# Optimization experiments

Measured on AMD Instinct MI355X. Metric: run time of the kernel, lower is better.

## Reference

```python
import jax, jax.numpy as jnp
import numpy as np
from jax import lax

FUSE_EPOCH = 9
STRIDE = (1, 1)
PAD = [(1, 1), (1, 1)]


def _conv_one(xi, ki):
    # xi: [ic, H, W], ki: [oc, ic, ks, ks] -> [oc, H', W']
    return lax.conv_general_dilated(
        xi[None], ki, window_strides=STRIDE, padding=PAD,
        dimension_numbers=("NCHW", "OIHW", "NCHW"))[0]


def setup_inputs() -> dict:
    key = jax.random.key(0)
    k1, k2, k3, k4 = jax.random.split(key, 4)
    B, IC, OC, KS, H, W, NDEMOG = 64, 64, 64, 3, 112, 112, 4
    x = jax.random.normal(k1, (B, IC, H, W), dtype=jnp.float32)
    fan_in = IC * KS * KS
    kernel_base = jax.random.normal(k2, (OC, IC, KS, KS), dtype=jnp.float32) / np.sqrt(fan_in)
    kernel_mask = jax.random.normal(k3, (NDEMOG, IC, KS, KS), dtype=jnp.float32)
    demog_label = jax.random.randint(k4, (B,), 0, NDEMOG, dtype=jnp.int64)
    return {"x": x, "kernel_base": kernel_base, "kernel_mask": kernel_mask,
            "demog_label": demog_label, "epoch": 0}


def reference(x, kernel_base, kernel_mask, demog_label, epoch):
    # Original: for each demog group d, conv samples with label d using
    # kernel_base * kernel_mask[d], scatter into output. Equivalent to a
    # per-sample kernel gathered by label (fuse_mark == -1 path uses mask 0
    # when epoch >= fuse_epoch).
    if epoch >= FUSE_EPOCH:
        idx = jnp.zeros_like(demog_label)
    else:
        idx = demog_label
    # per-sample kernels: [B, oc, ic, ks, ks]
    kernels = kernel_base[None] * kernel_mask[idx][:, None]
    return jax.vmap(_conv_one)(x, kernels)
```

## Files before the change

kernel.cpp:

```cpp
#include <hip/hip_runtime.h>
#include <hip/hip_bf16.h>


#define HH 112
#define WW 112
#define ICn 64
#define OCn 64
#define FUSE_EPOCH 9
#define NPIX (HH * WW)

typedef __attribute__((ext_vector_type(8)))  short  short8;
typedef __attribute__((ext_vector_type(8)))  unsigned short bf8;
typedef __attribute__((ext_vector_type(16))) float  f32x16;
typedef unsigned int u32;

#define WF_BYTES ((size_t)4 * 64 * 576 * 2)

static __device__ __forceinline__ unsigned short f2bf(float v) {
    __hip_bfloat16 hb = __float2bfloat16(v);
    return *reinterpret_cast<unsigned short*>(&hb);
}

static __device__ __forceinline__ void gload16(const unsigned short* g, unsigned short* l) {
    __builtin_amdgcn_global_load_lds(
        (const __attribute__((address_space(1))) u32*)g,
        (__attribute__((address_space(3))) u32*)l, 16, 0, 0);
}

__global__ __launch_bounds__(256)
void fuse_w_kernel(const float* __restrict__ kb, const float* __restrict__ km,
                   unsigned short* __restrict__ wf2)
{
    int idx = blockIdx.x * 256 + threadIdx.x;
    if (idx >= 4 * 4 * 9 * 2 * 64 * 8) return;
    int e  = idx & 7;
    int oc = (idx >> 3) & 63;
    int h  = (idx >> 9) & 1;
    int r  = idx >> 10;
    int t  = r % 9; r /= 9;
    int ck = r & 3;
    int d  = r >> 2;
    int ic = ck * 16 + h * 8 + e;
    wf2[idx] = f2bf(kb[(oc * ICn + ic) * 9 + t] * km[(d * ICn + ic) * 9 + t]);
}

__global__ __launch_bounds__(256, 2)
void adaconv_fused(const float* __restrict__ x,
                   const unsigned short* __restrict__ wf2,
                   const int* __restrict__ label,
                   const int* __restrict__ epoch,
                   float* __restrict__ out)
{
    __shared__ unsigned short Bb[2][10944];
    __shared__ unsigned short Ab[2][9216];

    const int tid  = threadIdx.x;
    const int b    = blockIdx.y;
    const int y0   = blockIdx.x * 4;
    const int w    = tid >> 6;
    const int lane = tid & 63;
    const int ln   = lane & 31;
    const int h    = lane >> 5;

    int d = (epoch[0] >= FUSE_EPOCH) ? 0 : label[b];
    d &= 3;
    const unsigned short* wfd = wf2 + (size_t)d * 36864;

    const float* ga[12];
    int  lbase[3];
    bool wact[3], gval[3];
    #pragma unroll
    for (int r = 0; r < 3; ++r) {
        int c = r * 256 + tid;
        bool a = (c < 672);
        int cc = a ? c : 671;
        int seg = cc % 28;
        int q   = cc / 28;
        int icq = q & 1;
        int rh  = q >> 1;
        int lr  = rh >> 1;
        int hh  = rh & 1;
        int gy  = y0 - 1 + lr;
        bool v  = ((unsigned)gy < 112u);
        wact[r] = a;
        gval[r] = v;
        lbase[r] = (rh * 114 + 4 * seg + 1) * 8 + icq * 4;
        int icl = hh * 8 + icq * 4;
        #pragma unroll
        for (int i = 0; i < 4; ++i)
            ga[r * 4 + i] = x + ((size_t)(b * 64 + icl + i) * 112 + (v ? gy : 0)) * 112 + 4 * seg;
    }

    auto issueA = [&](int buf, int ck1) {
        #pragma unroll
        for (int r = 0; r < 5; ++r) {
            int c = r * 256 + tid;
            if (c < 1152)
                gload16(wfd + ck1 * 9216 + (size_t)c * 8, &Ab[buf][(r * 256 + w * 64) * 8]);
        }
    };

    f32x16 acc[2][4];
    #pragma unroll
    for (int m = 0; m < 2; ++m)
        #pragma unroll
        for (int j = 0; j < 4; ++j)
            #pragma unroll
            for (int k = 0; k < 16; ++k) acc[m][j][k] = 0.f;

    const int bb = (w * 228 + h * 114 + ln) * 8;
    const int ab = h * 512 + ln * 8;

    if (tid < 48) {
        int bz = tid / 24, z = tid % 24;
        int rh = z >> 1, px = (z & 1) ? 113 : 0;
        bf8 zz = bf8{0,0,0,0,0,0,0,0};
        *reinterpret_cast<bf8*>(&Bb[bz][(rh * 114 + px) * 8]) = zz;
    }
    {
        float4 vl[12];
        #pragma unroll
        for (int r = 0; r < 3; ++r)
            if (wact[r])
                #pragma unroll
                for (int i = 0; i < 4; ++i)
                    vl[r * 4 + i] = *reinterpret_cast<const float4*>(ga[r * 4 + i]);
        issueA(0, 0);
        #pragma unroll
        for (int r = 0; r < 3; ++r) {
            if (!wact[r]) continue;
            float c0[4] = {vl[r*4+0].x, vl[r*4+0].y, vl[r*4+0].z, vl[r*4+0].w};
            float c1[4] = {vl[r*4+1].x, vl[r*4+1].y, vl[r*4+1].z, vl[r*4+1].w};
            float c2[4] = {vl[r*4+2].x, vl[r*4+2].y, vl[r*4+2].z, vl[r*4+2].w};
            float c3[4] = {vl[r*4+3].x, vl[r*4+3].y, vl[r*4+3].z, vl[r*4+3].w};
            #pragma unroll
            for (int p = 0; p < 4; ++p) {
                float f0 = gval[r] ? c0[p] : 0.f;
                float f1 = gval[r] ? c1[p] : 0.f;
                float f2 = gval[r] ? c2[p] : 0.f;
                float f3 = gval[r] ? c3[p] : 0.f;
                __hip_bfloat162 u01 = __float22bfloat162_rn(make_float2(f0, f1));
                __hip_bfloat162 u23 = __float22bfloat162_rn(make_float2(f2, f3));
                uint2 wv;
                wv.x = *reinterpret_cast<unsigned*>(&u01);
                wv.y = *reinterpret_cast<unsigned*>(&u23);
                *reinterpret_cast<uint2*>(&Bb[0][lbase[r] + p * 8]) = wv;
            }
        }
        __syncthreads();
    }

    #pragma unroll
    for (int ck = 0; ck < 4; ++ck) {
        const int cur = ck & 1, nxt = cur ^ 1;
        float4 vl[12];
        if (ck < 3) {
            #pragma unroll
            for (int r = 0; r < 3; ++r)
                if (wact[r])
                    #pragma unroll
                    for (int i = 0; i < 4; ++i)
                        vl[r * 4 + i] = *reinterpret_cast<const float4*>(
                            ga[r * 4 + i] + (size_t)(ck + 1) * 200704);
            issueA(nxt, ck + 1);
            __builtin_amdgcn_sched_barrier(0);
        }

        const unsigned short* Bc = Bb[cur];
        const unsigned short* Ac = Ab[cur];
        #pragma unroll
        for (int kh = 0; kh < 3; ++kh) {
            #pragma unroll
            for (int kw = 0; kw < 3; ++kw) {
                const int t = kh * 3 + kw;
                short8 a0 = *reinterpret_cast<const short8*>(&Ac[ab + t * 1024]);
                short8 a1 = *reinterpret_cast<const short8*>(&Ac[ab + 256 + t * 1024]);
                #pragma unroll
                for (int j = 0; j < 4; ++j) {
                    short8 bj = *reinterpret_cast<const short8*>(
                        &Bc[bb + (kh * 228 + kw + j * 32) * 8]);
                    acc[0][j] = __builtin_amdgcn_mfma_f32_32x32x16_bf16(a0, bj, acc[0][j], 0, 0, 0);
                    acc[1][j] = __builtin_amdgcn_mfma_f32_32x32x16_bf16(a1, bj, acc[1][j], 0, 0, 0);
                }
            }
        }

        if (ck < 3) {
            #pragma unroll
            for (int r = 0; r < 3; ++r) {
                if (!wact[r]) continue;
                float c0[4] = {vl[r*4+0].x, vl[r*4+0].y, vl[r*4+0].z, vl[r*4+0].w};
                float c1[4] = {vl[r*4+1].x, vl[r*4+1].y, vl[r*4+1].z, vl[r*4+1].w};
                float c2[4] = {vl[r*4+2].x, vl[r*4+2].y, vl[r*4+2].z, vl[r*4+2].w};
                float c3[4] = {vl[r*4+3].x, vl[r*4+3].y, vl[r*4+3].z, vl[r*4+3].w};
                #pragma unroll
                for (int p = 0; p < 4; ++p) {
                    float f0 = gval[r] ? c0[p] : 0.f;
                    float f1 = gval[r] ? c1[p] : 0.f;
                    float f2 = gval[r] ? c2[p] : 0.f;
                    float f3 = gval[r] ? c3[p] : 0.f;
                    __hip_bfloat162 u01 = __float22bfloat162_rn(make_float2(f0, f1));
                    __hip_bfloat162 u23 = __float22bfloat162_rn(make_float2(f2, f3));
                    uint2 wv;
                    wv.x = *reinterpret_cast<unsigned*>(&u01);
                    wv.y = *reinterpret_cast<unsigned*>(&u23);
                    *reinterpret_cast<uint2*>(&Bb[nxt][lbase[r] + p * 8]) = wv;
                }
            }
        }
        __syncthreads();
    }

    #pragma unroll
    for (int m = 0; m < 2; ++m) {
        #pragma unroll
        for (int j = 0; j < 4; ++j) {
            if (j == 3 && ln >= 16) continue;
            float* ob = out + ((size_t)(b * OCn + m * 32 + 4 * h)) * NPIX
                            + (y0 + w) * WW + j * 32 + ln;
            #pragma unroll
            for (int reg = 0; reg < 16; ++reg) {
                int row = (reg & 3) + 8 * (reg >> 2);
                ob[(size_t)row * NPIX] = acc[m][j][reg];
            }
        }
    }
}

#define ICP 24
#define WSTRIDE 152
__global__ __launch_bounds__(256, 2)
void adaconv_fallback(const float* __restrict__ x,
                      const float* __restrict__ kb,
                      const float* __restrict__ km,
                      const int* __restrict__ label,
                      const int* __restrict__ epoch,
                      float* __restrict__ out)
{
    __shared__ unsigned short Xs[18][34][ICP];
    __shared__ unsigned short Ws[64][WSTRIDE];

    const int tid = threadIdx.x;
    const int b   = blockIdx.y;
    const int bx  = blockIdx.x & 3;
    const int byy = blockIdx.x >> 2;
    const int x0 = bx * 32, y0 = byy * 16;

    int d = (epoch[0] >= FUSE_EPOCH) ? 0 : label[b];
    d &= 3;

    const int w    = tid >> 6;
    const int lane = tid & 63;
    const int ln   = lane & 31;
    const int h    = lane >> 5;

    f32x16 acc[2][4];
    #pragma unroll
    for (int m = 0; m < 2; ++m)
        #pragma unroll
        for (int j = 0; j < 4; ++j)
            #pragma unroll
            for (int k = 0; k < 16; ++k) acc[m][j][k] = 0.f;

    const float* xb = x + (size_t)b * ICn * HH * WW;

    for (int ck = 0; ck < 4; ++ck) {
        const int icb = ck * 16;
        __syncthreads();
        for (int idx = tid; idx < 18 * 34 * 16; idx += 256) {
            int ic  = idx / 612;
            int rem = idx - ic * 612;
            int r   = rem / 34;
            int c   = rem - r * 34;
            int gy = y0 - 1 + r, gx = x0 - 1 + c;
            float v = 0.f;
            if ((unsigned)gy < HH && (unsigned)gx < WW)
                v = xb[(size_t)(icb + ic) * (HH * WW) + gy * WW + gx];
            Xs[r][c][ic] = f2bf(v);
        }
        for (int i = tid; i < 9216; i += 256) {
            int ic_ = i & 15;
            int tt  = (i >> 4) % 9;
            int oc  = i / 144;
            int ic  = icb + ic_;
            Ws[oc][tt * 16 + ic_] = f2bf(kb[(oc * ICn + ic) * 9 + tt] * km[(d * ICn + ic) * 9 + tt]);
        }
        __syncthreads();
        #pragma unroll
        for (int kh = 0; kh < 3; ++kh)
            #pragma unroll
            for (int kw = 0; kw < 3; ++kw) {
                const int t = kh * 3 + kw;
                short8 a0 = *reinterpret_cast<const short8*>(&Ws[ln][t * 16 + h * 8]);
                short8 a1 = *reinterpret_cast<const short8*>(&Ws[32 + ln][t * 16 + h * 8]);
                #pragma unroll
                for (int rj = 0; rj < 4; ++rj) {
                    short8 bb2 = *reinterpret_cast<const short8*>(&Xs[4 * w + rj + kh][ln + kw][h * 8]);
                    acc[0][rj] = __builtin_amdgcn_mfma_f32_32x32x16_bf16(a0, bb2, acc[0][rj], 0, 0, 0);
                    acc[1][rj] = __builtin_amdgcn_mfma_f32_32x32x16_bf16(a1, bb2, acc[1][rj], 0, 0, 0);
                }
            }
    }

    const int xg = x0 + ln;
    if (xg < WW) {
        #pragma unroll
        for (int m = 0; m < 2; ++m)
            #pragma unroll
            for (int rj = 0; rj < 4; ++rj) {
                const int yg = y0 + 4 * w + rj;
                #pragma unroll
                for (int reg = 0; reg < 16; ++reg) {
                    const int row = (reg & 3) + 8 * (reg >> 2) + 4 * h;
                    out[(((size_t)b * OCn + m * 32 + row) * HH + yg) * WW + xg] = acc[m][rj][reg];
                }
            }
    }
}

extern "C" void kernel_launch(void* const* d_in, const int* in_sizes, int n_in,
                              void* d_out, int out_size, void* d_ws, size_t ws_size,
                              hipStream_t stream) {
    const float* x  = (const float*)d_in[0];
    const float* kb = (const float*)d_in[1];
    const float* km = (const float*)d_in[2];
    const int*   lb = (const int*)d_in[3];
    const int*   ep = (const int*)d_in[4];
    float* out = (float*)d_out;

    if (ws_size >= WF_BYTES) {
        unsigned short* wf2 = (unsigned short*)d_ws;
        fuse_w_kernel<<<576, 256, 0, stream>>>(kb, km, wf2);
        adaconv_fused<<<dim3(28, 64), 256, 0, stream>>>(x, wf2, lb, ep, out);
    } else {
        adaconv_fallback<<<dim3(28, 64), 256, 0, stream>>>(x, kb, km, lb, ep, out);
    }
}
```

Baseline: 119.4 us.

## Split input LDS tile into half-channel planes with vectorized 16-byte writes

Changes the LDS layout of the bf16 input tile. Each row is now split into two 4-channel planes, and the zero-padding column moves to slots 112/113, with lane 0 of the left tap redirected there. As a result, staging writes become two 16-byte stores per thread instead of four 8-byte stores. The MFMA B operand is now assembled from two 8-byte reads instead of one 16-byte read. It also refactors the conversion into a shared lambda. The aim is to cut LDS store instructions and bank conflicts during staging, at the cost of doubling LDS read instructions in the inner MFMA loop.

```diff
diff --git a/kernel.cpp b/kernel.cpp
--- a/kernel.cpp
+++ b/kernel.cpp
@@ -84,7 +84,8 @@
         bool v  = ((unsigned)gy < 112u);
         wact[r] = a;
         gval[r] = v;
-        lbase[r] = (rh * 114 + 4 * seg + 1) * 8 + icq * 4;
+        int rh2 = rh * 2 + icq;
+        lbase[r] = (rh2 * 114 + 4 * seg) * 4;
         int icl = hh * 8 + icq * 4;
         #pragma unroll
         for (int i = 0; i < 4; ++i)
@@ -100,32 +101,7 @@
         }
     };
 
-    f32x16 acc[2][4];
-    #pragma unroll
-    for (int m = 0; m < 2; ++m)
-        #pragma unroll
-        for (int j = 0; j < 4; ++j)
-            #pragma unroll
-            for (int k = 0; k < 16; ++k) acc[m][j][k] = 0.f;
-
-    const int bb = (w * 228 + h * 114 + ln) * 8;
-    const int ab = h * 512 + ln * 8;
-
-    if (tid < 48) {
-        int bz = tid / 24, z = tid % 24;
-        int rh = z >> 1, px = (z & 1) ? 113 : 0;
-        bf8 zz = bf8{0,0,0,0,0,0,0,0};
-        *reinterpret_cast<bf8*>(&Bb[bz][(rh * 114 + px) * 8]) = zz;
-    }
-    {
-        float4 vl[12];
-        #pragma unroll
-        for (int r = 0; r < 3; ++r)
-            if (wact[r])
-                #pragma unroll
-                for (int i = 0; i < 4; ++i)
-                    vl[r * 4 + i] = *reinterpret_cast<const float4*>(ga[r * 4 + i]);
-        issueA(0, 0);
+    auto writeB = [&](int buf, const float4* vl) {
         #pragma unroll
         for (int r = 0; r < 3; ++r) {
             if (!wact[r]) continue;
@@ -133,6 +109,7 @@
             float c1[4] = {vl[r*4+1].x, vl[r*4+1].y, vl[r*4+1].z, vl[r*4+1].w};
             float c2[4] = {vl[r*4+2].x, vl[r*4+2].y, vl[r*4+2].z, vl[r*4+2].w};
             float c3[4] = {vl[r*4+3].x, vl[r*4+3].y, vl[r*4+3].z, vl[r*4+3].w};
+            unsigned glo[4], ghi[4];
             #pragma unroll
             for (int p = 0; p < 4; ++p) {
                 float f0 = gval[r] ? c0[p] : 0.f;
@@ -141,14 +118,47 @@
                 float f3 = gval[r] ? c3[p] : 0.f;
                 __hip_bfloat162 u01 = __float22bfloat162_rn(make_float2(f0, f1));
                 __hip_bfloat162 u23 = __float22bfloat162_rn(make_float2(f2, f3));
-                uint2 wv;
-                wv.x = *reinterpret_cast<unsigned*>(&u01);
-                wv.y = *reinterpret_cast<unsigned*>(&u23);
-                *reinterpret_cast<uint2*>(&Bb[0][lbase[r] + p * 8]) = wv;
-            }
-        }
+                glo[p] = *reinterpret_cast<unsigned*>(&u01);
+                ghi[p] = *reinterpret_cast<unsigned*>(&u23);
+            }
+            uint4 w0 = make_uint4(glo[0], ghi[0], glo[1], ghi[1]);
+            uint4 w1 = make_uint4(glo[2], ghi[2], glo[3], ghi[3]);
+            *reinterpret_cast<uint4*>(&Bb[buf][lbase[r]])     = w0;
+            *reinterpret_cast<uint4*>(&Bb[buf][lbase[r] + 8]) = w1;
+        }
+    };
+
+    f32x16 acc[2][4];
+    #pragma unroll
+    for (int m = 0; m < 2; ++m)
+        #pragma unroll
+        for (int j = 0; j < 4; ++j)
+            #pragma unroll
+            for (int k = 0; k < 16; ++k) acc[m][j][k] = 0.f;
+
+    const int bB  = (4 * w + 2 * h) * 456;
+    const int ab  = h * 512 + ln * 8;
+    const int p00 = (ln == 0) ? 112 : (ln - 1);
+
+    if (tid < 96) {
+        int buf = tid / 48, z = tid % 48;
+        int rh2 = z >> 1, slot = 112 + (z & 1);
+        *reinterpret_cast<uint2*>(&Bb[buf][(rh2 * 114 + slot) * 4]) = make_uint2(0, 0);
+    }
+    {
+        float4 vl[12];
+        #pragma unroll
+        for (int r = 0; r < 3; ++r)
+            if (wact[r])
+                #pragma unroll
+                for (int i = 0; i < 4; ++i)
+                    vl[r * 4 + i] = *reinterpret_cast<const float4*>(ga[r * 4 + i]);
+        issueA(0, 0);
+        writeB(0, vl);
         __syncthreads();
     }
+
+    union U8 { short8 s; uint2 u2[2]; };
 
     #pragma unroll
     for (int ck = 0; ck < 4; ++ck) {
@@ -177,37 +187,19 @@
                 short8 a1 = *reinterpret_cast<const short8*>(&Ac[ab + 256 + t * 1024]);
                 #pragma unroll
                 for (int j = 0; j < 4; ++j) {
-                    short8 bj = *reinterpret_cast<const short8*>(
-                        &Bc[bb + (kh * 228 + kw + j * 32) * 8]);
-                    acc[0][j] = __builtin_amdgcn_mfma_f32_32x32x16_bf16(a0, bj, acc[0][j], 0, 0, 0);
-                    acc[1][j] = __builtin_amdgcn_mfma_f32_32x32x16_bf16(a1, bj, acc[1][j], 0, 0, 0);
+                    const int pxe = (j == 0 && kw == 0) ? p00 : (j * 32 + ln + kw - 1);
+                    U8 bj;
+                    bj.u2[0] = *reinterpret_cast<const uint2*>(
+                        &Bc[bB + kh * 1824 + pxe * 4]);
+                    bj.u2[1] = *reinterpret_cast<const uint2*>(
+                        &Bc[bB + kh * 1824 + 456 + pxe * 4]);
+                    acc[0][j] = __builtin_amdgcn_mfma_f32_32x32x16_bf16(a0, bj.s, acc[0][j], 0, 0, 0);
+                    acc[1][j] = __builtin_amdgcn_mfma_f32_32x32x16_bf16(a1, bj.s, acc[1][j], 0, 0, 0);
                 }
             }
         }
 
-        if (ck < 3) {
-            #pragma unroll
-            for (int r = 0; r < 3; ++r) {
-                if (!wact[r]) continue;
-                float c0[4] = {vl[r*4+0].x, vl[r*4+0].y, vl[r*4+0].z, vl[r*4+0].w};
-                float c1[4] = {vl[r*4+1].x, vl[r*4+1].y, vl[r*4+1].z, vl[r*4+1].w};
-                float c2[4] = {vl[r*4+2].x, vl[r*4+2].y, vl[r*4+2].z, vl[r*4+2].w};
-                float c3[4] = {vl[r*4+3].x, vl[r*4+3].y, vl[r*4+3].z, vl[r*4+3].w};
-                #pragma unroll
-                for (int p = 0; p < 4; ++p) {
-                    float f0 = gval[r] ? c0[p] : 0.f;
-                    float f1 = gval[r] ? c1[p] : 0.f;
-                    float f2 = gval[r] ? c2[p] : 0.f;
-                    float f3 = gval[r] ? c3[p] : 0.f;
-                    __hip_bfloat162 u01 = __float22bfloat162_rn(make_float2(f0, f1));
-                    __hip_bfloat162 u23 = __float22bfloat162_rn(make_float2(f2, f3));
-                    uint2 wv;
-                    wv.x = *reinterpret_cast<unsigned*>(&u01);
-                    wv.y = *reinterpret_cast<unsigned*>(&u23);
-                    *reinterpret_cast<uint2*>(&Bb[nxt][lbase[r] + p * 8]) = wv;
-                }
-            }
-        }
+        if (ck < 3) writeB(nxt, vl);
         __syncthreads();
     }
 
```

After: 251.3 us. 2.1x slower.
